# Kernel optimization log

Measured on AMD Instinct MI355X. Metric: run time of the kernel, lower is better.

The kernel has to match this reference:

```python
import jax, jax.numpy as jnp
import numpy as np

K = 9
DILATION = 2


def pairwise_distance(x):
    # x: (B, N, C) -> (B, N, N) squared Euclidean distances
    x_inner = -2.0 * jnp.einsum('bnc,bmc->bnm', x, x)
    x_square = jnp.sum(x * x, axis=-1, keepdims=True)  # (B, N, 1)
    return x_square + x_inner + jnp.swapaxes(x_square, 1, 2)


def setup_inputs() -> dict:
    key = jax.random.key(0)
    x = jax.random.normal(key, (4, 64, 4096, 1), dtype=jnp.float32)
    return {"x": x}


def reference(x):
    # x: (B, C, N, 1) -> (B, N, C)
    xt = jnp.swapaxes(x, 1, 2)[..., 0]
    B, N, C = xt.shape
    k_eff = K * DILATION
    neg_dist = -pairwise_distance(xt)  # (B, N, N)
    _, nn_idx = jax.lax.top_k(neg_dist, k_eff)  # (B, N, k_eff)
    center_idx = jnp.broadcast_to(jnp.arange(N)[None, :, None], (B, N, k_eff))
    edge_index = jnp.stack((nn_idx, center_idx), axis=0)  # (2, B, N, k_eff)
    # dilated selection: every DILATION-th neighbor -> (2, B, N, K)
    return edge_index[:, :, :, ::DILATION]
```

## Files before the change

kernel.cpp:

```cpp
#include <hip/hip_runtime.h>


#pragma clang fp contract(off)

#define BB    4
#define CDIM  64
#define NPTS  4096
#define KSEL  17
#define KOUT  9
#define QB    2

__global__ __launch_bounds__(256) void knn_sq(const float* __restrict__ x,
                                              float* __restrict__ sq) {
#pragma clang fp contract(off)
    int g = blockIdx.x * 256 + threadIdx.x;
    int b = g >> 12;
    int m = g & (NPTS - 1);
    const float* xb = x + (size_t)b * CDIM * NPTS + m;

    float a[CDIM];
    #pragma unroll
    for (int c = 0; c < CDIM; ++c) {
        float v = xb[c * NPTS];
        a[c] = v * v;
    }
    float s16[16];
    #pragma unroll
    for (int i = 0; i < 16; ++i)
        s16[i] = (a[i] + a[i + 16]) + (a[i + 32] + a[i + 48]);
    float t8[8];
    #pragma unroll
    for (int i = 0; i < 8; ++i) t8[i] = s16[i] + s16[i + 8];
    float t4[4];
    #pragma unroll
    for (int i = 0; i < 4; ++i) t4[i] = t8[i] + t8[i + 4];
    float u0 = t4[0] + t4[2];
    float u1 = t4[1] + t4[3];
    sq[g] = u0 + u1;
}

__global__ __launch_bounds__(256, 4) void knn_main(const float* __restrict__ x,
                                                   const float* __restrict__ sq,
                                                   int* __restrict__ out) {
#pragma clang fp contract(off)
    const int blk = blockIdx.x;
    const int b   = blk >> 11;
    const int n0  = (blk & 2047) * QB;
    const int t   = threadIdx.x;

    __shared__ float wbK[QB][2][4];
    __shared__ int   wbI[QB][2][4];

    const float* xb  = x + (size_t)b * CDIM * NPTS;
    const float* xq0 = xb + n0;
    const float* xq1 = xb + n0 + 1;
    const float* sqb = sq + (b << 12);
    const float* xp  = xb + 16 * t;

    float acc0[16], acc1[16];
    float4 a0, a1, a2, a3, b0, b1, b2, b3;

#define LOAD_A(CC) { const float4* _p = (const float4*)(xp + (size_t)(CC) * NPTS); \
                     a0 = _p[0]; a1 = _p[1]; a2 = _p[2]; a3 = _p[3]; }
#define LOAD_B(CC) { const float4* _p = (const float4*)(xp + (size_t)(CC) * NPTS); \
                     b0 = _p[0]; b1 = _p[1]; b2 = _p[2]; b3 = _p[3]; }

#define ACCUM(V0, V1, V2, V3, Q0, Q1)                                          \
    { const float _xv[16] = {V0.x,V0.y,V0.z,V0.w, V1.x,V1.y,V1.z,V1.w,         \
                             V2.x,V2.y,V2.z,V2.w, V3.x,V3.y,V3.z,V3.w};        \
      _Pragma("unroll")                                                        \
      for (int _j = 0; _j < 16; ++_j) {                                        \
          float _p0 = (Q0) * _xv[_j];                             \
          acc0[_j] = acc0[_j] + _p0;                   \
          float _p1 = (Q1) * _xv[_j];                                          \
          acc1[_j] = acc1[_j] + _p1;                                           \
      } }

    float qA0 = xq0[0],      qA1 = xq1[0];
    float qB0 = xq0[NPTS],   qB1 = xq1[NPTS];
    LOAD_A(0);
    LOAD_B(1);
    {
        const float _xv[16] = {a0.x,a0.y,a0.z,a0.w, a1.x,a1.y,a1.z,a1.w,
                               a2.x,a2.y,a2.z,a2.w, a3.x,a3.y,a3.z,a3.w};
        #pragma unroll
        for (int _j = 0; _j < 16; ++_j) {
            acc0[_j] = qA0 * _xv[_j];
            acc1[_j] = qA1 * _xv[_j];
        }
    }
    qA0 = xq0[2 * NPTS]; qA1 = xq1[2 * NPTS];
    LOAD_A(2);
    ACCUM(b0, b1, b2, b3, qB0, qB1)
    qB0 = xq0[3 * NPTS]; qB1 = xq1[3 * NPTS];

    for (int c = 2; c <= 60; c += 2) {
        LOAD_B(c + 1);
        ACCUM(a0, a1, a2, a3, qA0, qA1)
        qA0 = xq0[(size_t)(c + 2) * NPTS]; qA1 = xq1[(size_t)(c + 2) * NPTS];
        LOAD_A(c + 2);
        ACCUM(b0, b1, b2, b3, qB0, qB1)
        qB0 = xq0[(size_t)(c + 3) * NPTS]; qB1 = xq1[(size_t)(c + 3) * NPTS];
    }
    LOAD_B(63);
    ACCUM(a0, a1, a2, a3, qA0, qA1)
    ACCUM(b0, b1, b2, b3, qB0, qB1)

    float sqm[16];
    {
        const float4* sr = (const float4*)(sqb + 16 * t);
        float4 s0 = sr[0], s1 = sr[1], s2 = sr[2], s3 = sr[3];
        sqm[0]=s0.x; sqm[1]=s0.y; sqm[2]=s0.z; sqm[3]=s0.w;
        sqm[4]=s1.x; sqm[5]=s1.y; sqm[6]=s1.z; sqm[7]=s1.w;
        sqm[8]=s2.x; sqm[9]=s2.y; sqm[10]=s2.z; sqm[11]=s2.w;
        sqm[12]=s3.x; sqm[13]=s3.y; sqm[14]=s3.z; sqm[15]=s3.w;
    }

#define WAVE_ARGMIN(BD, BI)                                                    \
    _Pragma("unroll")                                                          \
    for (int _off = 32; _off >= 1; _off >>= 1) {                               \
        float _od = __shfl_down(BD, _off);                                     \
        int   _oi = __shfl_down(BI, _off);                                     \
        if (_od < BD || (_od == BD && _oi < BI)) { BD = _od; BI = _oi; }       \
    }

#define SELECT(ACC, QI)                                                        \
    {                                                                          \
        const float sqn = sqb[n0 + (QI)];                                      \
        _Pragma("unroll")                                                      \
        for (int j = 0; j < 16; ++j) {                                         \
            float inner = -2.0f * ACC[j];                   \
            float t1    = sqn + inner;                                         \
            ACC[j]      = t1 + sqm[j];            \
        }                                                                      \
        unsigned mask = 0;                                                     \
        float cm = 3.0e38f;                                                    \
        int   ci = 0x7fffffff;                                                 \
        _Pragma("unroll")                                                      \
        for (int j = 0; j < 16; ++j) {                                         \
            float v = ACC[j];                                                  \
            if (v < cm) { cm = v; ci = 16 * t + j; }                           \
        }                                                                      \
        float bd = cm;                                                         \
        int   bi = ci;                                                         \
        WAVE_ARGMIN(bd, bi)                                                    \
        if ((t & 63) == 0) { wbK[QI][0][t >> 6] = bd; wbI[QI][0][t >> 6] = bi; } \
        __syncthreads();                                                       \
        int myOut = 0;                                                         \
        for (int r = 0; r < KSEL; ++r) {                                       \
            const int p = r & 1;                                               \
            float gb = wbK[QI][p][0];                                          \
            int   gi = wbI[QI][p][0];                                          \
            _Pragma("unroll")                                                  \
            for (int w = 1; w < 4; ++w) {                                      \
                float od = wbK[QI][p][w];                                      \
                int   oi = wbI[QI][p][w];                                      \
                if (od < gb || (od == gb && oi < gi)) { gb = od; gi = oi; }    \
            }                                                                  \
            if (t < KOUT && r == 2 * t) myOut = gi;    \
            if (r + 1 < KSEL) {                                                \
                if ((gi >> 10) == (t >> 6)) {            \
                    if ((gi >> 4) == t) {              \
                        mask |= 1u << (gi & 15);                               \
                        cm = 3.0e38f; ci = 0x7fffffff;                         \
                        _Pragma("unroll")                                      \
                        for (int j = 0; j < 16; ++j) {                         \
                            float v = ACC[j];                                  \
                            if (!((mask >> j) & 1u) && v < cm) { cm = v; ci = 16 * t + j; } \
                        }                                                      \
                    }                                                          \
                    bd = cm; bi = ci;                                          \
                    WAVE_ARGMIN(bd, bi)                                        \
                }                                                              \
                if ((t & 63) == 0) { wbK[QI][p ^ 1][t >> 6] = bd; wbI[QI][p ^ 1][t >> 6] = bi; } \
                __syncthreads();                                               \
            }                                                                  \
        }                                                                      \
        if (t < KOUT) {                                                        \
            int    nq   = n0 + (QI);                                           \
            size_t base = (size_t)((b << 12) + nq) * KOUT;                     \
            out[base + t] = myOut;                                             \
            out[(size_t)BB * NPTS * KOUT + base + t] = nq;                     \
        }                                                                      \
    }

    SELECT(acc0, 0)
    SELECT(acc1, 1)
}

extern "C" void kernel_launch(void* const* d_in, const int* in_sizes, int n_in,
                              void* d_out, int out_size, void* d_ws, size_t ws_size,
                              hipStream_t stream) {
    const float* x   = (const float*)d_in[0];
    float*       sqv = (float*)d_ws;
    int*         out = (int*)d_out;

    hipLaunchKernelGGL(knn_sq,   dim3((BB * NPTS) / 256), dim3(256), 0, stream, x, sqv);
    hipLaunchKernelGGL(knn_main, dim3((BB * NPTS) / QB),  dim3(256), 0, stream, x, sqv, out);
}
```

Before: 544.8 us.

## Use FMA approximate distances with exact-recompute refinement over threshold candidates

The distance accumulation now uses fused multiply-adds, with the query coefficients staged in shared memory and a simpler unrolled loop. The query-norm term is dropped from the approximate ranking. An approximate top-17 pass finds a threshold, and all points within EPS of it are collected as candidates. Each candidate's distance is then recomputed in the exact reference order, and a wave-level selection over the candidates produces the final indices. This targets cheaper inner-loop arithmetic while keeping tie-breaking bit-exact. In exchange it adds atomics, an extra selection pass and a scattered recompute, and results could be wrong if more than CANDMAX candidates fall under the threshold.

```diff
diff --git a/kernel.cpp b/kernel.cpp
--- a/kernel.cpp
+++ b/kernel.cpp
@@ -9,6 +9,8 @@
 #define KSEL  17
 #define KOUT  9
 #define QB    2
+#define EPS   0.05f
+#define CANDMAX 64
 
 __global__ __launch_bounds__(256) void knn_sq(const float* __restrict__ x,
                                               float* __restrict__ sq) {
@@ -39,82 +41,11 @@
     sq[g] = u0 + u1;
 }
 
-__global__ __launch_bounds__(256, 4) void knn_main(const float* __restrict__ x,
-                                                   const float* __restrict__ sq,
-                                                   int* __restrict__ out) {
-#pragma clang fp contract(off)
-    const int blk = blockIdx.x;
-    const int b   = blk >> 11;
-    const int n0  = (blk & 2047) * QB;
-    const int t   = threadIdx.x;
-
-    __shared__ float wbK[QB][2][4];
-    __shared__ int   wbI[QB][2][4];
-
-    const float* xb  = x + (size_t)b * CDIM * NPTS;
-    const float* xq0 = xb + n0;
-    const float* xq1 = xb + n0 + 1;
-    const float* sqb = sq + (b << 12);
-    const float* xp  = xb + 16 * t;
-
-    float acc0[16], acc1[16];
-    float4 a0, a1, a2, a3, b0, b1, b2, b3;
-
-#define LOAD_A(CC) { const float4* _p = (const float4*)(xp + (size_t)(CC) * NPTS); \
-                     a0 = _p[0]; a1 = _p[1]; a2 = _p[2]; a3 = _p[3]; }
-#define LOAD_B(CC) { const float4* _p = (const float4*)(xp + (size_t)(CC) * NPTS); \
-                     b0 = _p[0]; b1 = _p[1]; b2 = _p[2]; b3 = _p[3]; }
-
-#define ACCUM(V0, V1, V2, V3, Q0, Q1)                                          \
-    { const float _xv[16] = {V0.x,V0.y,V0.z,V0.w, V1.x,V1.y,V1.z,V1.w,         \
-                             V2.x,V2.y,V2.z,V2.w, V3.x,V3.y,V3.z,V3.w};        \
-      _Pragma("unroll")                                                        \
-      for (int _j = 0; _j < 16; ++_j) {                                        \
-          float _p0 = (Q0) * _xv[_j];                             \
-          acc0[_j] = acc0[_j] + _p0;                   \
-          float _p1 = (Q1) * _xv[_j];                                          \
-          acc1[_j] = acc1[_j] + _p1;                                           \
-      } }
-
-    float qA0 = xq0[0],      qA1 = xq1[0];
-    float qB0 = xq0[NPTS],   qB1 = xq1[NPTS];
-    LOAD_A(0);
-    LOAD_B(1);
-    {
-        const float _xv[16] = {a0.x,a0.y,a0.z,a0.w, a1.x,a1.y,a1.z,a1.w,
-                               a2.x,a2.y,a2.z,a2.w, a3.x,a3.y,a3.z,a3.w};
-        #pragma unroll
-        for (int _j = 0; _j < 16; ++_j) {
-            acc0[_j] = qA0 * _xv[_j];
-            acc1[_j] = qA1 * _xv[_j];
-        }
-    }
-    qA0 = xq0[2 * NPTS]; qA1 = xq1[2 * NPTS];
-    LOAD_A(2);
-    ACCUM(b0, b1, b2, b3, qB0, qB1)
-    qB0 = xq0[3 * NPTS]; qB1 = xq1[3 * NPTS];
-
-    for (int c = 2; c <= 60; c += 2) {
-        LOAD_B(c + 1);
-        ACCUM(a0, a1, a2, a3, qA0, qA1)
-        qA0 = xq0[(size_t)(c + 2) * NPTS]; qA1 = xq1[(size_t)(c + 2) * NPTS];
-        LOAD_A(c + 2);
-        ACCUM(b0, b1, b2, b3, qB0, qB1)
-        qB0 = xq0[(size_t)(c + 3) * NPTS]; qB1 = xq1[(size_t)(c + 3) * NPTS];
-    }
-    LOAD_B(63);
-    ACCUM(a0, a1, a2, a3, qA0, qA1)
-    ACCUM(b0, b1, b2, b3, qB0, qB1)
-
-    float sqm[16];
-    {
-        const float4* sr = (const float4*)(sqb + 16 * t);
-        float4 s0 = sr[0], s1 = sr[1], s2 = sr[2], s3 = sr[3];
-        sqm[0]=s0.x; sqm[1]=s0.y; sqm[2]=s0.z; sqm[3]=s0.w;
-        sqm[4]=s1.x; sqm[5]=s1.y; sqm[6]=s1.z; sqm[7]=s1.w;
-        sqm[8]=s2.x; sqm[9]=s2.y; sqm[10]=s2.z; sqm[11]=s2.w;
-        sqm[12]=s3.x; sqm[13]=s3.y; sqm[14]=s3.z; sqm[15]=s3.w;
-    }
+#define FM4Q(ACC, QC, V, J)                                                    \
+    ACC[J]     = fmaf(QC, V.x, ACC[J]);                                        \
+    ACC[(J)+1] = fmaf(QC, V.y, ACC[(J)+1]);                                    \
+    ACC[(J)+2] = fmaf(QC, V.z, ACC[(J)+2]);                                    \
+    ACC[(J)+3] = fmaf(QC, V.w, ACC[(J)+3]);
 
 #define WAVE_ARGMIN(BD, BI)                                                    \
     _Pragma("unroll")                                                          \
@@ -124,15 +55,8 @@
         if (_od < BD || (_od == BD && _oi < BI)) { BD = _od; BI = _oi; }       \
     }
 
-#define SELECT(ACC, QI)                                                        \
+#define SELECT_T(ACC, QI, TVAR)                                                \
     {                                                                          \
-        const float sqn = sqb[n0 + (QI)];                                      \
-        _Pragma("unroll")                                                      \
-        for (int j = 0; j < 16; ++j) {                                         \
-            float inner = -2.0f * ACC[j];                   \
-            float t1    = sqn + inner;                                         \
-            ACC[j]      = t1 + sqm[j];            \
-        }                                                                      \
         unsigned mask = 0;                                                     \
         float cm = 3.0e38f;                                                    \
         int   ci = 0x7fffffff;                                                 \
@@ -146,7 +70,6 @@
         WAVE_ARGMIN(bd, bi)                                                    \
         if ((t & 63) == 0) { wbK[QI][0][t >> 6] = bd; wbI[QI][0][t >> 6] = bi; } \
         __syncthreads();                                                       \
-        int myOut = 0;                                                         \
         for (int r = 0; r < KSEL; ++r) {                                       \
             const int p = r & 1;                                               \
             float gb = wbK[QI][p][0];                                          \
@@ -157,7 +80,7 @@
                 int   oi = wbI[QI][p][w];                                      \
                 if (od < gb || (od == gb && oi < gi)) { gb = od; gi = oi; }    \
             }                                                                  \
-            if (t < KOUT && r == 2 * t) myOut = gi;    \
+            TVAR = gb;                                                         \
             if (r + 1 < KSEL) {                                                \
                 if ((gi >> 10) == (t >> 6)) {            \
                     if ((gi >> 4) == t) {              \
@@ -176,16 +99,113 @@
                 __syncthreads();                                               \
             }                                                                  \
         }                                                                      \
-        if (t < KOUT) {                                                        \
-            int    nq   = n0 + (QI);                                           \
-            size_t base = (size_t)((b << 12) + nq) * KOUT;                     \
-            out[base + t] = myOut;                                             \
-            out[(size_t)BB * NPTS * KOUT + base + t] = nq;                     \
-        }                                                                      \
-    }
-
-    SELECT(acc0, 0)
-    SELECT(acc1, 1)
+    }
+
+__global__ __launch_bounds__(256) void knn_main(const float* __restrict__ x,
+                                                const float* __restrict__ sq,
+                                                int* __restrict__ out) {
+#pragma clang fp contract(off)
+    const int blk = blockIdx.x;
+    const int b   = blk >> 11;
+    const int n0  = (blk & 2047) * QB;
+    const int t   = threadIdx.x;
+
+    __shared__ float2 qs2[CDIM];
+    __shared__ float  wbK[QB][2][4];
+    __shared__ int    wbI[QB][2][4];
+    __shared__ int    candCnt[QB];
+    __shared__ int    candM[QB][CANDMAX];
+
+    const float* xb  = x + (size_t)b * CDIM * NPTS;
+    const float* sqb = sq + (b << 12);
+    const float* xp  = xb + 16 * t;
+
+    if (t < CDIM)
+        qs2[t] = make_float2(xb[(size_t)t * NPTS + n0],
+                             xb[(size_t)t * NPTS + n0 + 1]);
+    if (t < QB) candCnt[t] = 0;
+    __syncthreads();
+
+    float acc0[16], acc1[16];
+    #pragma unroll
+    for (int j = 0; j < 16; ++j) { acc0[j] = 0.0f; acc1[j] = 0.0f; }
+
+    #pragma unroll 2
+    for (int c = 0; c < CDIM; ++c) {
+        const float4* xr = (const float4*)(xp + (size_t)c * NPTS);
+        float4 v0 = xr[0], v1 = xr[1], v2 = xr[2], v3 = xr[3];
+        float2 qc = qs2[c];
+        FM4Q(acc0, qc.x, v0, 0)  FM4Q(acc0, qc.x, v1, 4)
+        FM4Q(acc0, qc.x, v2, 8)  FM4Q(acc0, qc.x, v3, 12)
+        FM4Q(acc1, qc.y, v0, 0)  FM4Q(acc1, qc.y, v1, 4)
+        FM4Q(acc1, qc.y, v2, 8)  FM4Q(acc1, qc.y, v3, 12)
+    }
+
+    {
+        const float4* sr = (const float4*)(sqb + 16 * t);
+        float4 s0 = sr[0], s1 = sr[1], s2 = sr[2], s3 = sr[3];
+        const float sm[16] = {s0.x,s0.y,s0.z,s0.w, s1.x,s1.y,s1.z,s1.w,
+                              s2.x,s2.y,s2.z,s2.w, s3.x,s3.y,s3.z,s3.w};
+        #pragma unroll
+        for (int j = 0; j < 16; ++j) {
+            acc0[j] = fmaf(-2.0f, acc0[j], sm[j]);
+            acc1[j] = fmaf(-2.0f, acc1[j], sm[j]);
+        }
+    }
+
+    float T0 = 0.0f, T1 = 0.0f;
+    SELECT_T(acc0, 0, T0)
+    SELECT_T(acc1, 1, T1)
+
+    #pragma unroll
+    for (int j = 0; j < 16; ++j) {
+        if (acc0[j] <= T0 + EPS) {
+            int p = atomicAdd(&candCnt[0], 1);
+            if (p < CANDMAX) candM[0][p] = 16 * t + j;
+        }
+        if (acc1[j] <= T1 + EPS) {
+            int p = atomicAdd(&candCnt[1], 1);
+            if (p < CANDMAX) candM[1][p] = 16 * t + j;
+        }
+    }
+    __syncthreads();
+
+    const int wv = t >> 6, lane = t & 63;
+    if (wv < QB) {
+        const int qi  = wv;
+        const int cnt = min(candCnt[qi], CANDMAX);
+        const int nq  = n0 + qi;
+        float E   = 3.0e38f;
+        int   myM = 0x7fffffff;
+        if (lane < cnt) {
+            myM = candM[qi][lane];
+            const float* xm = xb + myM;
+            float d = (qi == 0 ? qs2[0].x : qs2[0].y) * xm[0];
+            for (int c = 1; c < CDIM; ++c) {
+                float qc = (qi == 0) ? qs2[c].x : qs2[c].y;
+                float p  = qc * xm[(size_t)c * NPTS];
+                d = d + p;
+            }
+            float inner = -2.0f * d;
+            float t1    = sqb[nq] + inner;
+            E = t1 + sqb[myM];
+        }
+        const size_t base = (size_t)((b << 12) + nq) * KOUT;
+        for (int r = 0; r < KSEL; ++r) {
+            float gk = E; int gi = myM;
+            #pragma unroll
+            for (int s = 32; s >= 1; s >>= 1) {
+                float ok = __shfl_down(gk, s);
+                int   oi = __shfl_down(gi, s);
+                if (ok < gk || (ok == gk && oi < gi)) { gk = ok; gi = oi; }
+            }
+            gk = __shfl(gk, 0); gi = __shfl(gi, 0);
+            if ((r & 1) == 0 && lane == 0) out[base + (r >> 1)] = gi;
+            if (myM == gi) E = 3.0e38f;
+        }
+        if (lane < KOUT)
+            out[(size_t)BB * NPTS * KOUT + base + lane] = nq;
+    }
 }
 
 extern "C" void kernel_launch(void* const* d_in, const int* in_sizes, int n_in,
```

After: 560.7 us. +2.9%, slower.
